# Kernel tuning notes

Measured on AMD Instinct MI355X. Metric: run time of the kernel, lower is better.

Reference implementation:

```python
import jax, jax.numpy as jnp
import numpy as np

DIM = 2048
HEADS = 16
DIM_HEAD = 128
FF_INNER = DIM * 4
SCALE_BASE = 512
EPS = 1e-5


def setup_inputs() -> dict:
    key = jax.random.key(0)
    k1, k2, k3, k4 = jax.random.split(key, 4)
    fused_out = HEADS * DIM_HEAD + DIM_HEAD + DIM_HEAD + 2 * FF_INNER  # 18688
    x = jax.random.normal(k1, (2, 2048, DIM), dtype=jnp.float32)
    gamma = jnp.ones((DIM,), dtype=jnp.float32)
    W_fused = jax.random.normal(k2, (DIM, fused_out), dtype=jnp.float32) * 0.02
    W_attn_out = jax.random.normal(k3, (HEADS * DIM_HEAD, DIM), dtype=jnp.float32) * 0.02
    W_ff_out = jax.random.normal(k4, (FF_INNER, DIM), dtype=jnp.float32) * 0.02
    return {"x": x, "gamma": gamma, "W_fused": W_fused, "W_attn_out": W_attn_out, "W_ff_out": W_ff_out}


def _rotate_half(t):
    t1, t2 = jnp.split(t, 2, axis=-1)
    return jnp.concatenate((-t2, t1), axis=-1)


def _rotary(n, dtype):
    # RotaryEmbedding with use_xpos=True, scale_base=512
    half = DIM_HEAD // 2
    inv_freq = 1.0 / (10000.0 ** (jnp.arange(0, DIM_HEAD, 2, dtype=dtype) / DIM_HEAD))
    t = jnp.arange(n, dtype=dtype)
    freqs = jnp.einsum('i,j->ij', t, inv_freq)          # [n, half]
    freqs = jnp.concatenate((freqs, freqs), axis=-1)    # [n, dh]
    scale_vec = (jnp.arange(0, DIM_HEAD, 2, dtype=dtype) + 0.4 * DIM_HEAD) / (1.4 * DIM_HEAD)
    power = (t - n // 2) / SCALE_BASE
    scale = scale_vec[None, :] ** power[:, None]        # [n, half]
    scale = jnp.concatenate((scale, scale), axis=-1)    # [n, dh]
    return freqs, scale


def _apply_rope(pos, t, scale):
    return t * jnp.cos(pos) * scale + _rotate_half(t) * jnp.sin(pos) * scale


def reference(x, gamma, W_fused, W_attn_out, W_ff_out):
    b, n, d = x.shape
    # LayerNorm (beta fixed at zero)
    mu = jnp.mean(x, axis=-1, keepdims=True)
    var = jnp.var(x, axis=-1, keepdims=True)
    xn = (x - mu) * jax.lax.rsqrt(var + EPS) * gamma

    proj = xn @ W_fused
    attn_inner = HEADS * DIM_HEAD
    q = proj[..., :attn_inner]
    k = proj[..., attn_inner:attn_inner + DIM_HEAD]
    v = proj[..., attn_inner + DIM_HEAD:attn_inner + 2 * DIM_HEAD]
    ff = proj[..., attn_inner + 2 * DIM_HEAD:]

    q = q.reshape(b, n, HEADS, DIM_HEAD).transpose(0, 2, 1, 3)  # b h n d

    pos, scale = _rotary(n, x.dtype)
    q = _apply_rope(pos, q, scale)            # broadcasts [n,dh] over b,h
    k = _apply_rope(pos, k, 1.0 / scale)      # k is [b, n, dh]

    # multi-query attention, causal
    sim = jnp.einsum('bhid,bjd->bhij', q, k) * (DIM_HEAD ** -0.5)
    causal_mask = jnp.triu(jnp.ones((n, n), dtype=bool), 1)
    sim = jnp.where(causal_mask, jnp.finfo(sim.dtype).min, sim)
    attn = jax.nn.softmax(sim, axis=-1)
    out = jnp.einsum('bhij,bjd->bhid', attn, v)
    out = out.transpose(0, 2, 1, 3).reshape(b, n, attn_inner)
    attn_out = out @ W_attn_out

    # SwiGLU: chunk -> silu(gate) * x
    ff_x, ff_gate = jnp.split(ff, 2, axis=-1)
    ff_out = (jax.nn.silu(ff_gate) * ff_x) @ W_ff_out

    return attn_out + ff_out
```

## Files before the change

### kernel.cpp

```cpp
#include <hip/hip_runtime.h>

typedef __attribute__((ext_vector_type(8))) short short8;
typedef __attribute__((ext_vector_type(4))) float floatx4;
typedef __attribute__((ext_vector_type(8))) unsigned short ushort8;
typedef __attribute__((ext_vector_type(2))) unsigned int uint2v;

#define FOUT 18688
#define FFI  8192
#define CATW 10240

__device__ __forceinline__ float b2f(unsigned short u){
  union { unsigned int i; float f; } v; v.i = ((unsigned int)u) << 16; return v.f;
}
__device__ __forceinline__ unsigned short f2b(float f){
  union { float f; unsigned int i; } v; v.f = f;
  unsigned int r = v.i + 0x7FFFu + ((v.i >> 16) & 1u);
  return (unsigned short)(r >> 16);
}
__device__ __forceinline__ void gld_lds16(const void* g, void* l){
  __builtin_amdgcn_global_load_lds((const __attribute__((address_space(1))) void*)g,
                                   (__attribute__((address_space(3))) void*)l, 16, 0, 0);
}

#define SCHED0() __builtin_amdgcn_sched_barrier(0)
#define BARR()   do{ SCHED0(); __builtin_amdgcn_s_barrier(); SCHED0(); }while(0)

__global__ __launch_bounds__(256) void ln_kernel(const float* __restrict__ x,
                                                 const float* __restrict__ gamma,
                                                 unsigned short* __restrict__ xn){
  int row = blockIdx.x;
  const float* xr = x + (size_t)row * 2048;
  int tid = threadIdx.x;
  float v[8]; float s = 0.f, s2 = 0.f;
#pragma unroll
  for(int i=0;i<8;i++){ float t = xr[tid + i*256]; v[i]=t; s+=t; s2+=t*t; }
#pragma unroll
  for(int off=32; off>=1; off>>=1){ s += __shfl_down(s, off, 64); s2 += __shfl_down(s2, off, 64); }
  __shared__ float red[8];
  int wv = tid>>6, ln_ = tid&63;
  if(ln_==0){ red[wv] = s; red[wv+4] = s2; }
  __syncthreads();
  s  = red[0]+red[1]+red[2]+red[3];
  s2 = red[4]+red[5]+red[6]+red[7];
  float mu  = s * (1.f/2048.f);
  float var = s2 * (1.f/2048.f) - mu*mu;
  float rstd = rsqrtf(var + 1e-5f);
#pragma unroll
  for(int i=0;i<8;i++){
    float o = (v[i]-mu)*rstd*gamma[tid + i*256];
    xn[(size_t)row*2048 + tid + i*256] = f2b(o);
  }
}

__global__ void tcast_kernel(const float* __restrict__ W, unsigned short* __restrict__ Wt,
                             int R, int C, int S, int O){
  __shared__ float t[32][33];
  int bx = blockIdx.x*32, by = blockIdx.y*32;
  int tx = threadIdx.x, ty = threadIdx.y;
#pragma unroll
  for(int i=0;i<4;i++) t[ty+i*8][tx] = W[(size_t)(by+ty+i*8)*C + bx+tx];
  __syncthreads();
#pragma unroll
  for(int i=0;i<4;i++) Wt[(size_t)(bx+ty+i*8)*S + O + by+tx] = f2b(t[tx][ty+i*8]);
}

__global__ void vtrans_kernel(const unsigned short* __restrict__ proj, unsigned short* __restrict__ vt){
  __shared__ unsigned short t[32][33];
  int b = blockIdx.z;
  int n0 = blockIdx.x*32, d0 = blockIdx.y*32;
  int tx = threadIdx.x, ty = threadIdx.y;
#pragma unroll
  for(int i=0;i<4;i++) t[ty+i*8][tx] = proj[(size_t)(b*2048 + n0+ty+i*8)*FOUT + 2176 + d0+tx];
  __syncthreads();
#pragma unroll
  for(int i=0;i<4;i++) vt[((size_t)b*128 + d0+ty+i*8)*2048 + n0+tx] = t[tx][ty+i*8];
}

__global__ __launch_bounds__(256) void rope_tab_kernel(floatx4* __restrict__ tab){
  int idx = blockIdx.x*256 + threadIdx.x;
  int i = idx >> 6, j = idx & 63;
  float fj = (float)j, fi = (float)i;
  float p = fi * powf(10000.f, -fj*(1.f/64.f));
  float c = cosf(p), s = sinf(p);
  float sv = (2.f*fj + 51.2f) * (1.f/179.2f);
  float pw = (fi - 1024.f) * (1.f/512.f);
  float sc = powf(sv, pw);
  const float att = 0.08838834764831843f;
  floatx4 o; o[0]=c*sc*att; o[1]=s*sc*att; o[2]=c/sc; o[3]=s/sc;
  tab[idx] = o;
}

__global__ __launch_bounds__(256) void rope_kernel(unsigned short* __restrict__ proj,
                                                   const floatx4* __restrict__ tab){
  int row = blockIdx.x;
  int i = row & 2047;
  unsigned short* pr = proj + (size_t)row*FOUT;
  for(int item = threadIdx.x; item < 17*64; item += 256){
    int slot = item >> 6;
    int j = item & 63;
    floatx4 t = tab[i*64 + j];
    float cs = (slot==16) ? t[2] : t[0];
    float ss = (slot==16) ? t[3] : t[1];
    int colbase = (slot<16) ? slot*128 : 2048;
    float x1 = b2f(pr[colbase+j]);
    float x2 = b2f(pr[colbase+j+64]);
    pr[colbase+j]    = f2b(x1*cs - x2*ss);
    pr[colbase+j+64] = f2b(x2*cs + x1*ss);
  }
}

template<int MODE>
__global__ __launch_bounds__(512, 2) void gemm8p_kernel(const unsigned short* __restrict__ A,
                                                        const unsigned short* __restrict__ Bt,
                                                        unsigned short* __restrict__ Cb,
                                                        float* __restrict__ Cf,
                                                        int N, int K, int NT, size_t zstride){
  __shared__ unsigned short lds[65536];
  const int tid = threadIdx.x;
  const int wave = tid>>6, lane = tid&63;
  const int l15 = lane&15, l4 = lane>>4;
  const int wr = wave>>2, wc = wave&3;
  int id = blockIdx.x;
  int cpx = (int)gridDim.x >> 3;
  int swz = (id & 7)*cpx + (id >> 3);
  int tm = swz & 15, tn = swz >> 4;
  int kbase = (int)blockIdx.z * (NT*64);
  const unsigned short* Ab = A  + (size_t)tm*256*K + kbase;
  const unsigned short* Bb = Bt + (size_t)tn*256*K + kbase;
  if(MODE==1) Cf += (size_t)blockIdx.z * zstride;

  const int r0 = tid>>3;
  const int colc = ((tid&7) ^ (r0&7))*8;
  const int dstw = wave*512;

#define STAGE(t_, h_, isB_) do{ \
    const unsigned short* g_ = (isB_) ? Bb : Ab; \
    int db_ = (((t_)&1)<<15) + ((isB_)<<14) + ((h_)<<13) + dstw; \
    gld_lds16(g_ + (size_t)((h_)*128 + r0)*K + (t_)*64 + colc, &lds[db_]); \
    gld_lds16(g_ + (size_t)((h_)*128 + r0 + 64)*K + (t_)*64 + colc, &lds[db_ + 4096]); \
  }while(0)

  const int sw8 = l15&7;
  const int fo0 = ((l4    )^sw8)*8;
  const int fo1 = ((l4 + 4)^sw8)*8;
  const int albase = (wr*128 + l15)*64;
  const int blbase = 16384 + (wc*64 + l15)*64;

#define RD_A(buf_, mh_, mf_, kk_) a_[(mf_)*2+(kk_)] = *(const short8*)&lds[(buf_) + albase + (mh_)*4096 + (mf_)*1024 + ((kk_)?fo1:fo0)]
#define RD_B(buf_, nf_, kk_)      b_[(nf_)*2+(kk_)]  = *(const short8*)&lds[(buf_) + blbase + (nf_)*1024 + ((kk_)?fo1:fo0)]
#define MFMA_Q(mo_, no_) do{ \
  _Pragma("unroll") for(int mf=0; mf<4; mf++) \
  _Pragma("unroll") for(int nf=0; nf<2; nf++) \
  _Pragma("unroll") for(int kk=0; kk<2; kk++) \
    acc[(mo_)*4+mf][(no_)*2+nf] = __builtin_amdgcn_mfma_f32_16x16x32_bf16( \
      a_[mf*2+kk], b_[((no_)*2+nf)*2+kk], acc[(mo_)*4+mf][(no_)*2+nf], 0,0,0); \
}while(0)

  floatx4 acc[8][4];
#pragma unroll
  for(int i=0;i<8;i++)
#pragma unroll
    for(int j=0;j<4;j++) acc[i][j] = (floatx4)0.f;

  STAGE(0,0,0); STAGE(0,1,0); STAGE(0,0,1); STAGE(0,1,1);
  STAGE(1,0,1); STAGE(1,1,1); STAGE(1,0,0);
  asm volatile("s_waitcnt vmcnt(6)" ::: "memory");
  BARR();

  short8 a_[8], b_[8];
  for(int t=0; t<NT; ++t){
    const int bufo = (t&1)<<15;
#pragma unroll
    for(int mf=0; mf<4; mf++){ RD_A(bufo,0,mf,0); RD_A(bufo,0,mf,1); }
#pragma unroll
    for(int nf=0; nf<4; nf++){ RD_B(bufo,nf,0); RD_B(bufo,nf,1); }
    if(t+1 < NT) STAGE(t+1,1,0);
    BARR();
    asm volatile("s_waitcnt lgkmcnt(0)" ::: "memory");
    SCHED0();
    __builtin_amdgcn_s_setprio(1);
    MFMA_Q(0,0);
    __builtin_amdgcn_s_setprio(0);
    BARR();
    if(t+2 < NT) STAGE(t+2,0,1);
    BARR();
    __builtin_amdgcn_s_setprio(1);
    MFMA_Q(0,1);
    __builtin_amdgcn_s_setprio(0);
    BARR();
#pragma unroll
    for(int mf=0; mf<4; mf++){ RD_A(bufo,1,mf,0); RD_A(bufo,1,mf,1); }
    if(t+2 < NT) STAGE(t+2,1,1);
    BARR();
    asm volatile("s_waitcnt lgkmcnt(0)" ::: "memory");
    SCHED0();
    __builtin_amdgcn_s_setprio(1);
    MFMA_Q(1,0);
    __builtin_amdgcn_s_setprio(0);
    BARR();
    if(t+2 < NT){
      STAGE(t+2,0,0);
      asm volatile("s_waitcnt vmcnt(6)" ::: "memory");
    } else if(t+1 < NT){
      asm volatile("s_waitcnt vmcnt(0)" ::: "memory");
    }
    SCHED0();
    BARR();
    __builtin_amdgcn_s_setprio(1);
    MFMA_Q(1,1);
    __builtin_amdgcn_s_setprio(0);
    SCHED0();
    BARR();
  }

#pragma unroll
  for(int m=0;m<8;m++){
#pragma unroll
    for(int n=0;n<4;n++){
#pragma unroll
      for(int r=0;r<4;r++){
        size_t row = (size_t)tm*256 + wr*128 + (m>>2)*64 + (m&3)*16 + l4*4 + r;
        size_t col = (size_t)tn*256 + wc*64 + n*16 + l15;
        float v = acc[m][n][r];
        if(MODE==0)      Cb[row*N + col] = f2b(v);
        else             Cf[row*N + col] = v;
      }
    }
  }
}

__global__ __launch_bounds__(256) void add2_kernel(const float* __restrict__ p0,
                                                   const float* __restrict__ p1,
                                                   float* __restrict__ o, int n4){
  for(int i = blockIdx.x*256 + threadIdx.x; i < n4; i += gridDim.x*256){
    floatx4 a = ((const floatx4*)p0)[i];
    floatx4 b = ((const floatx4*)p1)[i];
    ((floatx4*)o)[i] = a + b;
  }
}

__global__ __launch_bounds__(512) void attn_kernel(const unsigned short* __restrict__ proj,
                                                   const unsigned short* __restrict__ vt,
                                                   unsigned short* __restrict__ ao){
  __shared__ unsigned short lK[64*128];
  __shared__ unsigned short lV[128*64];
  __shared__ unsigned short lP[8*16*64];
  int qt = (int)gridDim.x - 1 - (int)blockIdx.x;
  int hh = blockIdx.y, b = blockIdx.z;
  int tid = threadIdx.x, wave = tid>>6, lane = tid&63;
  int l15 = lane&15, l4 = lane>>4;
  int q0 = qt*128;
  int qrow = q0 + wave*16 + l15;
  const unsigned short* qp = proj + (size_t)(b*2048 + qrow)*FOUT + hh*128 + l4*8;
  short8 qf[4];
#pragma unroll
  for(int ds=0; ds<4; ds++) qf[ds] = *(const short8*)(qp + ds*32);
  floatx4 po[8];
#pragma unroll
  for(int dt=0; dt<8; dt++) po[dt] = (floatx4)0.f;
  float mrun[4] = {-1e30f,-1e30f,-1e30f,-1e30f};
  float lrun[4] = {0.f,0.f,0.f,0.f};
  unsigned short* lPw = lP + wave*1024;
  const unsigned short* kb = proj + (size_t)(b*2048)*FOUT + 2048;
  const unsigned short* vb = vt + (size_t)b*128*2048;
  int kvmax = 2*qt + 1;

  for(int kv=0; kv<=kvmax; kv++){
    int kv0 = kv*64;
#pragma unroll
    for(int it=0; it<2; it++){
      int f = it*512 + tid;
      int r = f>>4, pc = f&15;
      int gc = pc ^ (r&7);
      gld_lds16(kb + (size_t)(kv0 + r)*FOUT + gc*8, &lK[(it*512 + wave*64)*8]);
    }
#pragma unroll
    for(int it=0; it<2; it++){
      int f = it*512 + tid;
      int d = f>>3, pc = f&7;
      int gc = pc ^ (d&7);
      gld_lds16(vb + (size_t)d*2048 + kv0 + gc*8, &lV[(it*512 + wave*64)*8]);
    }
    __syncthreads();
    floatx4 sa[4];
#pragma unroll
    for(int jt=0;jt<4;jt++) sa[jt] = (floatx4)0.f;
#pragma unroll
    for(int jt=0;jt<4;jt++){
      int krow = jt*16 + l15;
#pragma unroll
      for(int ds=0; ds<4; ds++){
        int pc = (l4 + ds*4) ^ (krow&7);
        short8 kf = *(const short8*)&lK[krow*128 + pc*8];
        sa[jt] = __builtin_amdgcn_mfma_f32_16x16x32_bf16(qf[ds], kf, sa[jt], 0,0,0);
      }
    }
    float pv[4][4];
    bool diag = (kv0 + 63 > q0 + wave*16);
#pragma unroll
    for(int jt=0;jt<4;jt++){
#pragma unroll
      for(int r=0;r<4;r++){
        float s = sa[jt][r];
        if(diag && (kv0 + jt*16 + l15 > q0 + wave*16 + l4*4 + r)) s = -1e30f;
        pv[jt][r] = s;
      }
    }
    float mnew[4], corr[4];
#pragma unroll
    for(int r=0;r<4;r++){
      float mx = fmaxf(fmaxf(pv[0][r],pv[1][r]),fmaxf(pv[2][r],pv[3][r]));
      mx = fmaxf(mx, __shfl_xor(mx, 1, 64));
      mx = fmaxf(mx, __shfl_xor(mx, 2, 64));
      mx = fmaxf(mx, __shfl_xor(mx, 4, 64));
      mx = fmaxf(mx, __shfl_xor(mx, 8, 64));
      float mn = fmaxf(mrun[r], mx);
      corr[r] = __expf(mrun[r] - mn);
      mrun[r] = mn;
      mnew[r] = mn;
    }
    float rsum[4] = {0.f,0.f,0.f,0.f};
#pragma unroll
    for(int jt=0;jt<4;jt++){
#pragma unroll
      for(int r=0;r<4;r++){
        float p = __expf(pv[jt][r] - mnew[r]);
        pv[jt][r] = p;
        rsum[r] += p;
      }
    }
#pragma unroll
    for(int r=0;r<4;r++){
      float rs = rsum[r];
      rs += __shfl_xor(rs, 1, 64);
      rs += __shfl_xor(rs, 2, 64);
      rs += __shfl_xor(rs, 4, 64);
      rs += __shfl_xor(rs, 8, 64);
      lrun[r] = lrun[r]*corr[r] + rs;
    }
#pragma unroll
    for(int dt=0;dt<8;dt++){
#pragma unroll
      for(int r=0;r<4;r++) po[dt][r] *= corr[r];
    }
#pragma unroll
    for(int jt=0;jt<4;jt++){
#pragma unroll
      for(int r=0;r<4;r++){
        int i_ = l4*4 + r;
        int j = jt*16 + l15;
        int pc = (j>>3) ^ (i_&7);
        lPw[i_*64 + pc*8 + (j&7)] = f2b(pv[jt][r]);
      }
    }
    asm volatile("s_waitcnt lgkmcnt(0)" ::: "memory");
    short8 pf[2];
#pragma unroll
    for(int ks=0;ks<2;ks++){
      int pc = (l4 + ks*4) ^ (l15&7);
      pf[ks] = *(const short8*)&lPw[l15*64 + pc*8];
    }
#pragma unroll
    for(int dt=0;dt<8;dt++){
      int d = dt*16 + l15;
#pragma unroll
      for(int ks=0;ks<2;ks++){
        int pc = (ks*4 + l4) ^ (d&7);
        short8 vf = *(const short8*)&lV[d*64 + pc*8];
        po[dt] = __builtin_amdgcn_mfma_f32_16x16x32_bf16(pf[ks], vf, po[dt], 0,0,0);
      }
    }
    __syncthreads();
  }
#pragma unroll
  for(int r=0;r<4;r++){
    float inv = 1.f / lrun[r];
    size_t orow = (size_t)(b*2048 + q0 + wave*16 + l4*4 + r);
#pragma unroll
    for(int dt=0;dt<8;dt++){
      ao[orow*CATW + hh*128 + dt*16 + l15] = f2b(po[dt][r]*inv);
    }
  }
}

__global__ __launch_bounds__(256) void swiglu_kernel(const unsigned short* __restrict__ proj,
                                                     unsigned short* __restrict__ cat){
  size_t idx = (size_t)blockIdx.x*256 + threadIdx.x;
  int row = (int)(idx >> 10);
  int c8  = (int)(idx & 1023);
  const unsigned short* pr = proj + (size_t)row*FOUT + 2304 + c8*8;
  ushort8 xv = *(const ushort8*)pr;
  ushort8 gv = *(const ushort8*)(pr + FFI);
  ushort8 ov;
#pragma unroll
  for(int e=0;e<8;e++){
    float xf = b2f(xv[e]);
    float gf = b2f(gv[e]);
    float sg = gf / (1.f + __expf(-gf));
    ov[e] = f2b(sg*xf);
  }
  *(ushort8*)(cat + (size_t)row*CATW + 2048 + c8*8) = ov;
}

extern "C" void kernel_launch(void* const* d_in, const int* in_sizes, int n_in,
                              void* d_out, int out_size, void* d_ws, size_t ws_size,
                              hipStream_t stream){
  const float* x     = (const float*)d_in[0];
  const float* gamma = (const float*)d_in[1];
  const float* Wf    = (const float*)d_in[2];
  const float* Wa    = (const float*)d_in[3];
  const float* Wff   = (const float*)d_in[4];
  float* out = (float*)d_out;

  char* p = (char*)d_ws;
  unsigned short* xn    = (unsigned short*)p;  p += (size_t)4096*2048*2;
  unsigned short* WfT   = (unsigned short*)p;  p += (size_t)18688*2048*2;
  unsigned short* proj  = (unsigned short*)p;  p += (size_t)4096*18688*2;
  unsigned short* BtCat = (unsigned short*)p;  p += (size_t)2048*CATW*2;
  unsigned short* cat   = (unsigned short*)p;  p += (size_t)4096*CATW*2;
  unsigned short* vtb   = (unsigned short*)p;  p += (size_t)2*128*2048*2;
  floatx4*        rtab  = (floatx4*)p;         p += (size_t)2048*64*16;
  float* part = (float*)d_ws;

  ln_kernel<<<4096, 256, 0, stream>>>(x, gamma, xn);
  rope_tab_kernel<<<512, 256, 0, stream>>>(rtab);
  tcast_kernel<<<dim3(584,64),  dim3(32,8), 0, stream>>>(Wf,  WfT,   2048, 18688, 2048, 0);
  tcast_kernel<<<dim3(64,64),   dim3(32,8), 0, stream>>>(Wa,  BtCat, 2048, 2048,  CATW, 0);
  tcast_kernel<<<dim3(64,256),  dim3(32,8), 0, stream>>>(Wff, BtCat, 8192, 2048,  CATW, 2048);
  gemm8p_kernel<0><<<dim3(1168,1,1), 512, 0, stream>>>(xn, WfT, proj, nullptr, 18688, 2048, 32, 0);
  rope_kernel<<<4096, 256, 0, stream>>>(proj, rtab);
  vtrans_kernel<<<dim3(64,4,2), dim3(32,8), 0, stream>>>(proj, vtb);
  attn_kernel<<<dim3(16,16,2), 512, 0, stream>>>(proj, vtb, cat);
  swiglu_kernel<<<16384, 256, 0, stream>>>(proj, cat);
  gemm8p_kernel<1><<<dim3(128,1,2), 512, 0, stream>>>(cat, BtCat, nullptr, part, 2048, 10240, 80,
                                                      (size_t)4096*2048);
  add2_kernel<<<2048, 256, 0, stream>>>(part, part + (size_t)4096*2048, out, 2097152);
}
```

Measured before the change: 769.9 us.

## Vectorize weight transpose-cast and split GEMM LDS fragment reads per k-half

Replaces the 32x32 transpose-cast kernel with a 64x64 tile version that uses 16-byte float4 loads and 16-byte bf16x8 stores, to cut memory transactions when converting the weights. The GEMM main loop now reads A and B fragments in k-half chunks just before each MFMA quarter, with separate register arrays and extra lgkmcnt waits. This interleaves LDS reads with MFMA work and changes register pressure. The extra waits could also add stalls.

```diff
diff --git a/kernel.cpp b/kernel.cpp
--- a/kernel.cpp
+++ b/kernel.cpp
@@ -3,7 +3,6 @@
 typedef __attribute__((ext_vector_type(8))) short short8;
 typedef __attribute__((ext_vector_type(4))) float floatx4;
 typedef __attribute__((ext_vector_type(8))) unsigned short ushort8;
-typedef __attribute__((ext_vector_type(2))) unsigned int uint2v;
 
 #define FOUT 18688
 #define FFI  8192
@@ -52,16 +51,30 @@
   }
 }
 
-__global__ void tcast_kernel(const float* __restrict__ W, unsigned short* __restrict__ Wt,
-                             int R, int C, int S, int O){
-  __shared__ float t[32][33];
-  int bx = blockIdx.x*32, by = blockIdx.y*32;
-  int tx = threadIdx.x, ty = threadIdx.y;
-#pragma unroll
-  for(int i=0;i<4;i++) t[ty+i*8][tx] = W[(size_t)(by+ty+i*8)*C + bx+tx];
+__global__ __launch_bounds__(256) void tcast64_kernel(const float* __restrict__ W,
+                                                      unsigned short* __restrict__ Wt,
+                                                      int C, int S, int O){
+  __shared__ float t[64][65];
+  int bx = blockIdx.x*64;
+  int by = blockIdx.y*64;
+  int tid = threadIdx.x;
+  int r = tid>>2, cq = (tid&3)*16;
+  const float* src = W + (size_t)(by + r)*C + bx + cq;
+#pragma unroll
+  for(int e=0;e<4;e++){
+    floatx4 v = *(const floatx4*)(src + e*4);
+    t[r][cq+e*4+0]=v[0]; t[r][cq+e*4+1]=v[1]; t[r][cq+e*4+2]=v[2]; t[r][cq+e*4+3]=v[3];
+  }
   __syncthreads();
 #pragma unroll
-  for(int i=0;i<4;i++) Wt[(size_t)(bx+ty+i*8)*S + O + by+tx] = f2b(t[tx][ty+i*8]);
+  for(int it=0; it<2; it++){
+    int s_ = it*256 + tid;
+    int c = s_>>3, j8 = s_&7;
+    ushort8 o;
+#pragma unroll
+    for(int e=0;e<8;e++) o[e] = f2b(t[j8*8+e][c]);
+    *(ushort8*)&Wt[(size_t)(bx+c)*S + O + by + j8*8] = o;
+  }
 }
 
 __global__ void vtrans_kernel(const unsigned short* __restrict__ proj, unsigned short* __restrict__ vt){
@@ -146,15 +159,17 @@
   const int albase = (wr*128 + l15)*64;
   const int blbase = 16384 + (wc*64 + l15)*64;
 
-#define RD_A(buf_, mh_, mf_, kk_) a_[(mf_)*2+(kk_)] = *(const short8*)&lds[(buf_) + albase + (mh_)*4096 + (mf_)*1024 + ((kk_)?fo1:fo0)]
-#define RD_B(buf_, nf_, kk_)      b_[(nf_)*2+(kk_)]  = *(const short8*)&lds[(buf_) + blbase + (nf_)*1024 + ((kk_)?fo1:fo0)]
-#define MFMA_Q(mo_, no_) do{ \
+#define RD_A4(arr_, buf_, mh_, fo_) do{ \
   _Pragma("unroll") for(int mf=0; mf<4; mf++) \
-  _Pragma("unroll") for(int nf=0; nf<2; nf++) \
-  _Pragma("unroll") for(int kk=0; kk<2; kk++) \
-    acc[(mo_)*4+mf][(no_)*2+nf] = __builtin_amdgcn_mfma_f32_16x16x32_bf16( \
-      a_[mf*2+kk], b_[((no_)*2+nf)*2+kk], acc[(mo_)*4+mf][(no_)*2+nf], 0,0,0); \
-}while(0)
+    arr_[mf] = *(const short8*)&lds[(buf_) + albase + (mh_)*4096 + mf*1024 + (fo_)]; }while(0)
+#define RD_B4(arr_, buf_, fo_) do{ \
+  _Pragma("unroll") for(int nf=0; nf<4; nf++) \
+    arr_[nf] = *(const short8*)&lds[(buf_) + blbase + nf*1024 + (fo_)]; }while(0)
+#define MFMA_P(aarr_, barr_, mh_) do{ \
+  _Pragma("unroll") for(int mf=0; mf<4; mf++) \
+  _Pragma("unroll") for(int nf=0; nf<4; nf++) \
+    acc[(mh_)*4+mf][nf] = __builtin_amdgcn_mfma_f32_16x16x32_bf16( \
+      aarr_[mf], barr_[nf], acc[(mh_)*4+mf][nf], 0,0,0); }while(0)
 
   floatx4 acc[8][4];
 #pragma unroll
@@ -167,37 +182,39 @@
   asm volatile("s_waitcnt vmcnt(6)" ::: "memory");
   BARR();
 
-  short8 a_[8], b_[8];
+  short8 a00_[4], a01_[4], a10_[4], a11_[4], b0_[4], b1_[4];
   for(int t=0; t<NT; ++t){
     const int bufo = (t&1)<<15;
-#pragma unroll
-    for(int mf=0; mf<4; mf++){ RD_A(bufo,0,mf,0); RD_A(bufo,0,mf,1); }
-#pragma unroll
-    for(int nf=0; nf<4; nf++){ RD_B(bufo,nf,0); RD_B(bufo,nf,1); }
+    RD_A4(a00_, bufo, 0, fo0);
+    RD_B4(b0_,  bufo, fo0);
     if(t+1 < NT) STAGE(t+1,1,0);
     BARR();
     asm volatile("s_waitcnt lgkmcnt(0)" ::: "memory");
     SCHED0();
     __builtin_amdgcn_s_setprio(1);
-    MFMA_Q(0,0);
+    MFMA_P(a00_, b0_, 0);
     __builtin_amdgcn_s_setprio(0);
     BARR();
+    RD_A4(a01_, bufo, 0, fo1);
+    RD_B4(b1_,  bufo, fo1);
     if(t+2 < NT) STAGE(t+2,0,1);
     BARR();
+    asm volatile("s_waitcnt lgkmcnt(0)" ::: "memory");
+    SCHED0();
     __builtin_amdgcn_s_setprio(1);
-    MFMA_Q(0,1);
+    MFMA_P(a01_, b1_, 0);
     __builtin_amdgcn_s_setprio(0);
     BARR();
-#pragma unroll
-    for(int mf=0; mf<4; mf++){ RD_A(bufo,1,mf,0); RD_A(bufo,1,mf,1); }
+    RD_A4(a10_, bufo, 1, fo0);
     if(t+2 < NT) STAGE(t+2,1,1);
     BARR();
     asm volatile("s_waitcnt lgkmcnt(0)" ::: "memory");
     SCHED0();
     __builtin_amdgcn_s_setprio(1);
-    MFMA_Q(1,0);
+    MFMA_P(a10_, b0_, 1);
     __builtin_amdgcn_s_setprio(0);
     BARR();
+    RD_A4(a11_, bufo, 1, fo1);
     if(t+2 < NT){
       STAGE(t+2,0,0);
       asm volatile("s_waitcnt vmcnt(6)" ::: "memory");
@@ -206,8 +223,10 @@
     }
     SCHED0();
     BARR();
+    asm volatile("s_waitcnt lgkmcnt(0)" ::: "memory");
+    SCHED0();
     __builtin_amdgcn_s_setprio(1);
-    MFMA_Q(1,1);
+    MFMA_P(a11_, b1_, 1);
     __builtin_amdgcn_s_setprio(0);
     SCHED0();
     BARR();
@@ -424,9 +443,9 @@
 
   ln_kernel<<<4096, 256, 0, stream>>>(x, gamma, xn);
   rope_tab_kernel<<<512, 256, 0, stream>>>(rtab);
-  tcast_kernel<<<dim3(584,64),  dim3(32,8), 0, stream>>>(Wf,  WfT,   2048, 18688, 2048, 0);
-  tcast_kernel<<<dim3(64,64),   dim3(32,8), 0, stream>>>(Wa,  BtCat, 2048, 2048,  CATW, 0);
-  tcast_kernel<<<dim3(64,256),  dim3(32,8), 0, stream>>>(Wff, BtCat, 8192, 2048,  CATW, 2048);
+  tcast64_kernel<<<dim3(292,32),  256, 0, stream>>>(Wf,  WfT,   18688, 2048, 0);
+  tcast64_kernel<<<dim3(32,32),   256, 0, stream>>>(Wa,  BtCat, 2048,  CATW, 0);
+  tcast64_kernel<<<dim3(32,128),  256, 0, stream>>>(Wff, BtCat, 2048,  CATW, 2048);
   gemm8p_kernel<0><<<dim3(1168,1,1), 512, 0, stream>>>(xn, WfT, proj, nullptr, 18688, 2048, 32, 0);
   rope_kernel<<<4096, 256, 0, stream>>>(proj, rtab);
   vtrans_kernel<<<dim3(64,4,2), dim3(32,8), 0, stream>>>(proj, vtb);
```

Result: no change. 756.8 us (-1.7%).
